# Kernel optimization log

Hardware: AMD Instinct MI355X
Metric: run time of the kernel (lower is better)

Reference implementation:

```python
import jax, jax.numpy as jnp
import numpy as np

NUM_JOINTS = 24
NUM_THETAS = NUM_JOINTS * 3  # 72
NUM_VERTS = 6890
NUM_BETAS = 10
BATCH = 512

SMPL_PARENTS = np.array([0, 0, 0, 0, 1, 2, 3, 4, 5, 6, 7, 8, 9, 9, 9,
                         12, 13, 14, 16, 17, 18, 19, 20, 21], dtype=np.int32)


def setup_inputs() -> dict:
    key = jax.random.key(0)
    ks = jax.random.split(key, 6)
    x = jax.random.normal(ks[0], (BATCH, NUM_THETAS + NUM_BETAS), dtype=jnp.float32) * 0.3
    v_template = jax.random.normal(ks[1], (NUM_VERTS, 3), dtype=jnp.float32) * 0.3
    shapedirs = jax.random.normal(ks[2], (NUM_BETAS, NUM_VERTS * 3), dtype=jnp.float32) * 0.01
    posedirs = jax.random.normal(ks[3], (207, NUM_VERTS * 3), dtype=jnp.float32) * 0.001
    Jr = jax.random.uniform(ks[4], (NUM_VERTS, NUM_JOINTS), dtype=jnp.float32)
    J_regressor = Jr / jnp.sum(Jr, axis=0, keepdims=True)
    W = jax.random.uniform(ks[5], (NUM_VERTS, NUM_JOINTS), dtype=jnp.float32)
    lbs_weights = W / jnp.sum(W, axis=1, keepdims=True)  # rows sum to 1 (skinning weights)
    parents = jnp.asarray(SMPL_PARENTS)
    return {"x": x, "v_template": v_template, "shapedirs": shapedirs,
            "J_regressor": J_regressor, "posedirs": posedirs,
            "lbs_weights": lbs_weights, "parents": parents}


def batch_rodrigues(theta):
    # theta: [N,3] axis-angle -> [N,3,3] rotation matrices
    angle = jnp.linalg.norm(theta + 1e-8, axis=1, keepdims=True)  # [N,1]
    r = theta / angle                                              # [N,3] unit axis
    cos = jnp.cos(angle)[..., None]                                # [N,1,1]
    sin = jnp.sin(angle)[..., None]
    outer = r[:, :, None] * r[:, None, :]                          # [N,3,3]
    rx, ry, rz = r[:, 0], r[:, 1], r[:, 2]
    zero = jnp.zeros_like(rx)
    K = jnp.stack([zero, -rz, ry,
                   rz, zero, -rx,
                   -ry, rx, zero], axis=1).reshape(-1, 3, 3)       # skew-symmetric
    eye = jnp.eye(3, dtype=theta.dtype)
    return cos * eye + (1.0 - cos) * outer + sin * K


def global_rigid_transformation(Rs, J, parents):
    # Rs: [B,24,3,3], J: [B,24,3] -> A: [B,24,4,4]
    B = Rs.shape[0]
    dtype = Rs.dtype
    bottom = jnp.broadcast_to(jnp.array([0, 0, 0, 1], dtype=dtype), (B, 1, 4))

    def make_A(R, t):  # R:[B,3,3], t:[B,3]
        Rt = jnp.concatenate([R, t[:, :, None]], axis=2)  # [B,3,4]
        return jnp.concatenate([Rt, bottom], axis=1)       # [B,4,4]

    parents = np.asarray(parents)
    results = [make_A(Rs[:, 0], J[:, 0])]
    for i in range(1, NUM_JOINTS):
        t_rel = J[:, i] - J[:, parents[i]]
        A_here = make_A(Rs[:, i], t_rel)
        results.append(jnp.matmul(results[parents[i]], A_here))
    results = jnp.stack(results, axis=1)  # [B,24,4,4]

    Js_w0 = jnp.concatenate([J, jnp.zeros((B, NUM_JOINTS, 1), dtype=dtype)], axis=2)  # [B,24,4]
    init_bone = jnp.einsum('bjpq,bjq->bjp', results, Js_w0)                           # [B,24,4]
    A = results - jnp.pad(init_bone[..., None], ((0, 0), (0, 0), (0, 0), (3, 0)))
    return A


def reference(x, v_template, shapedirs, J_regressor, posedirs, lbs_weights, parents):
    B = x.shape[0]
    thetas = x[:, :NUM_THETAS]
    betas = x[:, NUM_THETAS:]

    # shape blendshapes
    v_shaped = (betas @ shapedirs).reshape(B, NUM_VERTS, 3) + v_template  # [B,V,3]

    J = jnp.einsum('bvc,vj->bjc', v_shaped, J_regressor)  # [B,24,3]

    # pose rotations + pose blendshapes
    Rs = batch_rodrigues(thetas.reshape(-1, 3)).reshape(B, NUM_JOINTS, 3, 3)
    pose_feature = (Rs[:, 1:] - jnp.eye(3, dtype=x.dtype)).reshape(B, 207)
    v_posed = (pose_feature @ posedirs).reshape(B, NUM_VERTS, 3) + v_shaped

    # kinematic chain
    A = global_rigid_transformation(Rs, J, parents)  # [B,24,4,4]

    # linear blend skinning
    T = jnp.einsum('vj,bjpq->bvpq', lbs_weights, A)  # [B,V,4,4]
    v_posed_homo = jnp.concatenate(
        [v_posed, jnp.ones((B, NUM_VERTS, 1), dtype=x.dtype)], axis=2)  # [B,V,4]
    verts = jnp.einsum('bvpq,bvq->bvp', T, v_posed_homo)[:, :, :3]
    return verts
```

## Files before the change

kernel.cpp:

```cpp
#include <hip/hip_runtime.h>

#define NUM_JOINTS 24
#define NUM_VERTS  6890
#define NUM_COORDS (NUM_VERTS * 3)
#define NUM_BETAS  10
#define KTOT       217
#define KPAD       224
#define BATCH      512
#define NPAD       20672
#define DPAD       20736
#define VPAD       6912

#define WS_SJ   0
#define WS_JT   720
#define WS_XBF  800
#define WS_DBF  58144
#define WS_WHBF 2380576
#define WS_AH   2491168
#define WS_AL   2622240
#define WS_JRT  2753312

typedef __attribute__((ext_vector_type(8))) short short8;
typedef __attribute__((ext_vector_type(4))) float f32x4;

__device__ inline unsigned short f2bf(float f) {
    union { float f; unsigned u; } c; c.f = f;
    unsigned u = c.u;
    u += 0x7fffu + ((u >> 16) & 1u);
    return (unsigned short)(u >> 16);
}
__device__ inline float bf2f(unsigned short h) {
    union { unsigned u; float f; } c; c.u = ((unsigned)h) << 16;
    return c.f;
}

__global__ __launch_bounds__(256) void prep_vert(const float* __restrict__ Jr,
                                                 const float* __restrict__ w,
                                                 float* __restrict__ jrT,
                                                 unsigned short* __restrict__ whbf) {
    const int v = blockIdx.x * 256 + threadIdx.x;
    if (v >= VPAD) return;
    const bool ok = (v < NUM_VERTS);
    #pragma unroll
    for (int j = 0; j < 24; ++j)
        jrT[j * VPAD + v] = ok ? Jr[v * 24 + j] : 0.f;
    unsigned short row[32];
    #pragma unroll
    for (int j = 0; j < 32; ++j)
        row[j] = f2bf((ok && j < 24) ? w[v * 24 + j] : 0.f);
    #pragma unroll
    for (int i = 0; i < 4; ++i)
        *(float4*)(whbf + (size_t)v * 32 + i * 8) = *(const float4*)(&row[i * 8]);
}

__global__ __launch_bounds__(256) void reduce_sj(const float* __restrict__ jrT,
                                                 const float* __restrict__ sd,
                                                 const float* __restrict__ vt,
                                                 float* __restrict__ ws) {
    const int s = blockIdx.x;
    const int j = blockIdx.y;
    const int tid = threadIdx.x;
    const float* jr = jrT + j * VPAD;
    float sum = 0.f;
    if (s < 30) {
        const int k = s / 3, c = s % 3;
        const float* src = sd + (size_t)k * NUM_COORDS;
        for (int v = tid; v < NUM_VERTS; v += 256)
            sum += jr[v] * src[v * 3 + c];
    } else {
        const int c = s - 30;
        for (int v = tid; v < NUM_VERTS; v += 256)
            sum += jr[v] * vt[v * 3 + c];
    }
    __shared__ float red[256];
    red[tid] = sum;
    __syncthreads();
    for (int off = 128; off > 0; off >>= 1) {
        if (tid < off) red[tid] += red[tid + off];
        __syncthreads();
    }
    if (tid == 0) {
        if (s < 30) ws[WS_SJ + (s / 3) * 72 + j * 3 + (s % 3)] = red[0];
        else        ws[WS_JT + j * 3 + (s - 30)] = red[0];
    }
}

__global__ __launch_bounds__(256) void convert_dbf(const float* __restrict__ sd,
                                                   const float* __restrict__ pd,
                                                   unsigned short* __restrict__ dbf) {
    const int c = blockIdx.x * 256 + threadIdx.x;
    const bool valid = (c < NUM_COORDS);
    unsigned short* drow = dbf + (size_t)c * KPAD;
    for (int g = 0; g < 4; ++g) {
        unsigned buf[28];
        #pragma unroll
        for (int h = 0; h < 28; ++h) {
            const int k0 = g * 56 + 2 * h;
            const int k1 = k0 + 1;
            float v0 = 0.f, v1 = 0.f;
            if (valid) {
                v0 = (k0 < 10) ? sd[(size_t)k0 * NUM_COORDS + c]
                   : (k0 < KTOT) ? pd[(size_t)(k0 - 10) * NUM_COORDS + c] : 0.f;
                v1 = (k1 < 10) ? sd[(size_t)k1 * NUM_COORDS + c]
                   : (k1 < KTOT) ? pd[(size_t)(k1 - 10) * NUM_COORDS + c] : 0.f;
            }
            buf[h] = (unsigned)f2bf(v0) | ((unsigned)f2bf(v1) << 16);
        }
        #pragma unroll
        for (int h = 0; h < 7; ++h)
            *(float4*)(drow + g * 56 + h * 8) = *(const float4*)(&buf[h * 4]);
    }
}

__global__ __launch_bounds__(64) void per_batch(const float* __restrict__ x,
                                                const int* __restrict__ parents,
                                                const float* __restrict__ ws_sj,
                                                unsigned short* __restrict__ ahi,
                                                unsigned short* __restrict__ alo,
                                                unsigned short* __restrict__ xbf) {
    const int b = blockIdx.x;
    const int tid = threadIdx.x;
    __shared__ float Rs[24][9], Jl[24][3], Rg[24][9], tg[24][3], As[24][12];
    const float* row = x + b * (NUM_BETAS + 72);

    if (tid < 24) {
        const int j = tid;
        const float t0 = row[3 * j + 0], t1 = row[3 * j + 1], t2 = row[3 * j + 2];
        const float a0 = t0 + 1e-8f, a1 = t1 + 1e-8f, a2 = t2 + 1e-8f;
        const float angle = sqrtf(a0 * a0 + a1 * a1 + a2 * a2);
        const float inv = 1.0f / angle;
        const float rx = t0 * inv, ry = t1 * inv, rz = t2 * inv;
        const float c = cosf(angle), sn = sinf(angle), o = 1.f - c;
        float R[9];
        R[0] = c + o * rx * rx;       R[1] = o * rx * ry - sn * rz; R[2] = o * rx * rz + sn * ry;
        R[3] = o * rx * ry + sn * rz; R[4] = c + o * ry * ry;       R[5] = o * ry * rz - sn * rx;
        R[6] = o * rx * rz - sn * ry; R[7] = o * ry * rz + sn * rx; R[8] = c + o * rz * rz;
        #pragma unroll
        for (int i = 0; i < 9; ++i) Rs[j][i] = R[i];
        #pragma unroll
        for (int c3 = 0; c3 < 3; ++c3) {
            float s = ws_sj[WS_JT + j * 3 + c3];
            #pragma unroll
            for (int k = 0; k < NUM_BETAS; ++k)
                s += row[72 + k] * ws_sj[WS_SJ + k * 72 + j * 3 + c3];
            Jl[j][c3] = s;
        }
        if (j >= 1) {
            #pragma unroll
            for (int i = 0; i < 9; ++i) {
                const float pf = R[i] - ((i == 0 || i == 4 || i == 8) ? 1.f : 0.f);
                xbf[(size_t)b * KPAD + 10 + (j - 1) * 9 + i] = f2bf(pf);
            }
        }
    }
    if (tid < NUM_BETAS) xbf[(size_t)b * KPAD + tid] = f2bf(row[72 + tid]);
    if (tid == 63) {
        #pragma unroll
        for (int k = KTOT; k < KPAD; ++k) xbf[(size_t)b * KPAD + k] = 0;
    }
    __syncthreads();

    if (tid == 0) {
        #pragma unroll
        for (int i = 0; i < 9; ++i) Rg[0][i] = Rs[0][i];
        #pragma unroll
        for (int c3 = 0; c3 < 3; ++c3) tg[0][c3] = Jl[0][c3];
        for (int i = 1; i < 24; ++i) {
            const int p = parents[i];
            float tmp[9];
            #pragma unroll
            for (int r = 0; r < 3; ++r)
                #pragma unroll
                for (int cc = 0; cc < 3; ++cc)
                    tmp[r * 3 + cc] = Rg[p][r * 3 + 0] * Rs[i][0 + cc] +
                                      Rg[p][r * 3 + 1] * Rs[i][3 + cc] +
                                      Rg[p][r * 3 + 2] * Rs[i][6 + cc];
            #pragma unroll
            for (int q = 0; q < 9; ++q) Rg[i][q] = tmp[q];
            const float tr0 = Jl[i][0] - Jl[p][0];
            const float tr1 = Jl[i][1] - Jl[p][1];
            const float tr2 = Jl[i][2] - Jl[p][2];
            #pragma unroll
            for (int r = 0; r < 3; ++r)
                tg[i][r] = Rg[p][r * 3 + 0] * tr0 + Rg[p][r * 3 + 1] * tr1 +
                           Rg[p][r * 3 + 2] * tr2 + tg[p][r];
        }
    }
    __syncthreads();

    if (tid < 24) {
        const int j = tid;
        #pragma unroll
        for (int r = 0; r < 3; ++r) {
            const float t = tg[j][r] - (Rg[j][r * 3 + 0] * Jl[j][0] +
                                        Rg[j][r * 3 + 1] * Jl[j][1] +
                                        Rg[j][r * 3 + 2] * Jl[j][2]);
            As[j][r * 4 + 0] = Rg[j][r * 3 + 0];
            As[j][r * 4 + 1] = Rg[j][r * 3 + 1];
            As[j][r * 4 + 2] = Rg[j][r * 3 + 2];
            As[j][r * 4 + 3] = t;
        }
    }
    __syncthreads();

    if (tid < 32) {
        const int r = tid >> 1;
        const int half = tid & 1;
        unsigned short hi[16], lo[16];
        #pragma unroll
        for (int i = 0; i < 16; ++i) {
            const int j = half * 16 + i;
            float v = 0.f;
            if (r < 12 && j < 24) v = As[j][r];
            const unsigned short h = f2bf(v);
            hi[i] = h;
            lo[i] = f2bf(v - bf2f(h));
        }
        unsigned short* dh = ahi + ((size_t)b * 16 + r) * 32 + half * 16;
        unsigned short* dl = alo + ((size_t)b * 16 + r) * 32 + half * 16;
        #pragma unroll
        for (int i = 0; i < 2; ++i) {
            *(float4*)(dh + i * 8) = *(const float4*)(&hi[i * 8]);
            *(float4*)(dl + i * 8) = *(const float4*)(&lo[i * 8]);
        }
    }
}

__global__ __launch_bounds__(256) void gemm_mfma(const unsigned short* __restrict__ dbf,
                                                 const unsigned short* __restrict__ xbf,
                                                 const float* __restrict__ vt,
                                                 float* __restrict__ out) {
    __shared__ __align__(16) unsigned short Xs[64 * 232];
    const int tid  = threadIdx.x;
    const int wave = tid >> 6;
    const int lane = tid & 63;
    const int col  = lane & 15;
    const int quad = lane >> 4;
    const int n0   = blockIdx.x * 64;
    const int nc   = n0 + wave * 16 + col;

    short8 bfrag[7];
    {
        const unsigned short* brow = dbf + (size_t)nc * KPAD + quad * 8;
        #pragma unroll
        for (int kb = 0; kb < 7; ++kb)
            bfrag[kb] = *(const short8*)(brow + kb * 32);
    }
    const float vtl = (nc < NUM_COORDS) ? vt[nc] : 0.f;
    const bool nok = (nc < NUM_COORDS);

    for (int chunk = 0; chunk < 2; ++chunk) {
        const int m0 = blockIdx.y * 128 + chunk * 64;
        __syncthreads();
        #pragma unroll
        for (int i = 0; i < 7; ++i) {
            const int c = tid + i * 256;
            const int r = c / 28;
            const int off = c % 28;
            const float4 v = *(const float4*)(xbf + (size_t)(m0 + r) * KPAD + off * 8);
            *(float4*)(&Xs[r * 232 + off * 8]) = v;
        }
        __syncthreads();

        #pragma unroll
        for (int mt = 0; mt < 4; ++mt) {
            const unsigned short* arow = &Xs[(mt * 16 + col) * 232 + quad * 8];
            f32x4 acc = {0.f, 0.f, 0.f, 0.f};
            #pragma unroll
            for (int kb = 0; kb < 7; ++kb) {
                const short8 afrag = *(const short8*)(arow + kb * 32);
                acc = __builtin_amdgcn_mfma_f32_16x16x32_bf16(afrag, bfrag[kb], acc, 0, 0, 0);
            }
            if (nok) {
                float* base = out + (size_t)(m0 + mt * 16 + quad * 4) * NUM_COORDS + nc;
                base[0]                       = acc[0] + vtl;
                base[(size_t)NUM_COORDS]      = acc[1] + vtl;
                base[(size_t)2 * NUM_COORDS]  = acc[2] + vtl;
                base[(size_t)3 * NUM_COORDS]  = acc[3] + vtl;
            }
        }
    }
}

__global__ __launch_bounds__(256) void skin_mfma(const unsigned short* __restrict__ whbf,
                                                 const unsigned short* __restrict__ ahi,
                                                 const unsigned short* __restrict__ alo,
                                                 float* __restrict__ out) {
    __shared__ float Ts[4][64 * 17];
    const int tid  = threadIdx.x;
    const int wave = tid >> 6;
    const int lane = tid & 63;
    const int col  = lane & 15;
    const int quad = lane >> 4;
    const int v0   = blockIdx.x * 64;
    const int b0   = blockIdx.y * 32;

    short8 wfrag[4];
    #pragma unroll
    for (int mt = 0; mt < 4; ++mt)
        wfrag[mt] = *(const short8*)(whbf + (size_t)(v0 + mt * 16 + col) * 32 + quad * 8);

    float* ts = &Ts[wave][0];
    const int vv = v0 + lane;
    const bool vok = (vv < NUM_VERTS);

    for (int nt = wave; nt < 32; nt += 4) {
        const int b = b0 + nt;
        float* orow = out + (size_t)b * NUM_COORDS + (size_t)vv * 3;
        float h0 = 0.f, h1 = 0.f, h2 = 0.f;
        if (vok) { h0 = orow[0]; h1 = orow[1]; h2 = orow[2]; }

        const short8 bh = *(const short8*)(ahi + ((size_t)b * 16 + col) * 32 + quad * 8);
        const short8 bl = *(const short8*)(alo + ((size_t)b * 16 + col) * 32 + quad * 8);

        f32x4 acc[4];
        #pragma unroll
        for (int mt = 0; mt < 4; ++mt) {
            f32x4 z = {0.f, 0.f, 0.f, 0.f};
            z = __builtin_amdgcn_mfma_f32_16x16x32_bf16(wfrag[mt], bh, z, 0, 0, 0);
            z = __builtin_amdgcn_mfma_f32_16x16x32_bf16(wfrag[mt], bl, z, 0, 0, 0);
            acc[mt] = z;
        }
        #pragma unroll
        for (int mt = 0; mt < 4; ++mt)
            #pragma unroll
            for (int r = 0; r < 4; ++r)
                ts[(mt * 16 + quad * 4 + r) * 17 + col] = acc[mt][r];

        float Tp[12];
        #pragma unroll
        for (int i = 0; i < 12; ++i) Tp[i] = ts[lane * 17 + i];

        if (vok) {
            const float o0 = Tp[0] * h0 + Tp[1] * h1 + Tp[2]  * h2 + Tp[3];
            const float o1 = Tp[4] * h0 + Tp[5] * h1 + Tp[6]  * h2 + Tp[7];
            const float o2 = Tp[8] * h0 + Tp[9] * h1 + Tp[10] * h2 + Tp[11];
            orow[0] = o0; orow[1] = o1; orow[2] = o2;
        }
    }
}

extern "C" void kernel_launch(void* const* d_in, const int* in_sizes, int n_in,
                              void* d_out, int out_size, void* d_ws, size_t ws_size,
                              hipStream_t stream) {
    const float* x  = (const float*)d_in[0];
    const float* vt = (const float*)d_in[1];
    const float* sd = (const float*)d_in[2];
    const float* Jr = (const float*)d_in[3];
    const float* pd = (const float*)d_in[4];
    const float* w  = (const float*)d_in[5];
    const int* parents = (const int*)d_in[6];
    float* out = (float*)d_out;
    float* ws  = (float*)d_ws;
    unsigned short* xbf  = (unsigned short*)(ws + WS_XBF);
    unsigned short* dbf  = (unsigned short*)(ws + WS_DBF);
    unsigned short* whbf = (unsigned short*)(ws + WS_WHBF);
    unsigned short* ahi  = (unsigned short*)(ws + WS_AH);
    unsigned short* alo  = (unsigned short*)(ws + WS_AL);
    float* jrT = ws + WS_JRT;

    prep_vert  <<<27, 256, 0, stream>>>(Jr, w, jrT, whbf);
    convert_dbf<<<81, 256, 0, stream>>>(sd, pd, dbf);
    reduce_sj  <<<dim3(33, 24), 256, 0, stream>>>(jrT, sd, vt, ws);
    per_batch  <<<BATCH, 64, 0, stream>>>(x, parents, ws, ahi, alo, xbf);
    gemm_mfma  <<<dim3(323, 4), 256, 0, stream>>>(dbf, xbf, vt, out);
    skin_mfma  <<<dim3(108, 16), 256, 0, stream>>>(whbf, ahi, alo, out);
}
```

Measured before the change: 165.6 us.

## Fuse all stages into one cooperative persistent kernel with grid syncs

Replaces the six separate launches with a single cooperative kernel that runs the prep, per-batch, GEMM and skinning stages as tile loops separated by grid-wide syncs. Four non-cooperative kernels remain as a fallback. The joint-regressor transpose buffer is dropped, so the reduction now reads Jr directly with a strided access. The per-batch stage packs four batches into each 256-thread block. The aim is to remove launch gaps between stages, at the cost of grid.sync overhead, a grid size capped at 1024 blocks, and host-side occupancy and attribute queries on every call.

```diff
diff --git a/kernel.cpp b/kernel.cpp
--- a/kernel.cpp
+++ b/kernel.cpp
@@ -1,4 +1,7 @@
 #include <hip/hip_runtime.h>
+#include <hip/hip_cooperative_groups.h>
+
+namespace cg = cooperative_groups;
 
 #define NUM_JOINTS 24
 #define NUM_VERTS  6890
@@ -7,8 +10,6 @@
 #define KTOT       217
 #define KPAD       224
 #define BATCH      512
-#define NPAD       20672
-#define DPAD       20736
 #define VPAD       6912
 
 #define WS_SJ   0
@@ -18,7 +19,6 @@
 #define WS_WHBF 2380576
 #define WS_AH   2491168
 #define WS_AL   2622240
-#define WS_JRT  2753312
 
 typedef __attribute__((ext_vector_type(8))) short short8;
 typedef __attribute__((ext_vector_type(4))) float f32x4;
@@ -34,97 +34,103 @@
     return c.f;
 }
 
-__global__ __launch_bounds__(256) void prep_vert(const float* __restrict__ Jr,
-                                                 const float* __restrict__ w,
-                                                 float* __restrict__ jrT,
-                                                 unsigned short* __restrict__ whbf) {
-    const int v = blockIdx.x * 256 + threadIdx.x;
-    if (v >= VPAD) return;
-    const bool ok = (v < NUM_VERTS);
-    #pragma unroll
-    for (int j = 0; j < 24; ++j)
-        jrT[j * VPAD + v] = ok ? Jr[v * 24 + j] : 0.f;
-    unsigned short row[32];
-    #pragma unroll
-    for (int j = 0; j < 32; ++j)
-        row[j] = f2bf((ok && j < 24) ? w[v * 24 + j] : 0.f);
-    #pragma unroll
-    for (int i = 0; i < 4; ++i)
-        *(float4*)(whbf + (size_t)v * 32 + i * 8) = *(const float4*)(&row[i * 8]);
-}
-
-__global__ __launch_bounds__(256) void reduce_sj(const float* __restrict__ jrT,
-                                                 const float* __restrict__ sd,
-                                                 const float* __restrict__ vt,
-                                                 float* __restrict__ ws) {
-    const int s = blockIdx.x;
-    const int j = blockIdx.y;
-    const int tid = threadIdx.x;
-    const float* jr = jrT + j * VPAD;
-    float sum = 0.f;
-    if (s < 30) {
-        const int k = s / 3, c = s % 3;
-        const float* src = sd + (size_t)k * NUM_COORDS;
-        for (int v = tid; v < NUM_VERTS; v += 256)
-            sum += jr[v] * src[v * 3 + c];
+struct PBShm {
+    float Rs[4][24][9];
+    float Jl[4][24][3];
+    float Rg[4][24][9];
+    float tg[4][24][3];
+    float As[4][24][12];
+};
+
+
+__device__ __forceinline__ void tile_prep(int t, int tid,
+                                          const float* __restrict__ Jr,
+                                          const float* __restrict__ sd,
+                                          const float* __restrict__ pd,
+                                          const float* __restrict__ vt,
+                                          const float* __restrict__ w,
+                                          unsigned short* __restrict__ whbf,
+                                          unsigned short* __restrict__ dbf,
+                                          float* __restrict__ ws,
+                                          float* red) {
+    if (t < 27) {
+        const int v = t * 256 + tid;
+        const bool ok = (v < NUM_VERTS);
+        unsigned short row[32];
+        #pragma unroll
+        for (int j = 0; j < 32; ++j)
+            row[j] = f2bf((ok && j < 24) ? w[v * 24 + j] : 0.f);
+        #pragma unroll
+        for (int i = 0; i < 4; ++i)
+            *(float4*)(whbf + (size_t)v * 32 + i * 8) = *(const float4*)(&row[i * 8]);
+    } else if (t < 108) {
+        const int c = (t - 27) * 256 + tid;
+        const bool valid = (c < NUM_COORDS);
+        unsigned short* drow = dbf + (size_t)c * KPAD;
+        for (int g = 0; g < 4; ++g) {
+            unsigned buf[28];
+            #pragma unroll
+            for (int h = 0; h < 28; ++h) {
+                const int k0 = g * 56 + 2 * h;
+                const int k1 = k0 + 1;
+                float v0 = 0.f, v1 = 0.f;
+                if (valid) {
+                    v0 = (k0 < 10) ? sd[(size_t)k0 * NUM_COORDS + c]
+                       : (k0 < KTOT) ? pd[(size_t)(k0 - 10) * NUM_COORDS + c] : 0.f;
+                    v1 = (k1 < 10) ? sd[(size_t)k1 * NUM_COORDS + c]
+                       : (k1 < KTOT) ? pd[(size_t)(k1 - 10) * NUM_COORDS + c] : 0.f;
+                }
+                buf[h] = (unsigned)f2bf(v0) | ((unsigned)f2bf(v1) << 16);
+            }
+            #pragma unroll
+            for (int h = 0; h < 7; ++h)
+                *(float4*)(drow + g * 56 + h * 8) = *(const float4*)(&buf[h * 4]);
+        }
     } else {
-        const int c = s - 30;
-        for (int v = tid; v < NUM_VERTS; v += 256)
-            sum += jr[v] * vt[v * 3 + c];
-    }
-    __shared__ float red[256];
-    red[tid] = sum;
-    __syncthreads();
-    for (int off = 128; off > 0; off >>= 1) {
-        if (tid < off) red[tid] += red[tid + off];
+        const int u = t - 108;
+        const int s = u % 33;
+        const int j = u / 33;
+        float sum = 0.f;
+        if (s < 30) {
+            const int k = s / 3, c = s % 3;
+            const float* src = sd + (size_t)k * NUM_COORDS;
+            for (int v = tid; v < NUM_VERTS; v += 256)
+                sum += Jr[v * 24 + j] * src[v * 3 + c];
+        } else {
+            const int c = s - 30;
+            for (int v = tid; v < NUM_VERTS; v += 256)
+                sum += Jr[v * 24 + j] * vt[v * 3 + c];
+        }
+        red[tid] = sum;
         __syncthreads();
-    }
-    if (tid == 0) {
-        if (s < 30) ws[WS_SJ + (s / 3) * 72 + j * 3 + (s % 3)] = red[0];
-        else        ws[WS_JT + j * 3 + (s - 30)] = red[0];
-    }
-}
-
-__global__ __launch_bounds__(256) void convert_dbf(const float* __restrict__ sd,
-                                                   const float* __restrict__ pd,
-                                                   unsigned short* __restrict__ dbf) {
-    const int c = blockIdx.x * 256 + threadIdx.x;
-    const bool valid = (c < NUM_COORDS);
-    unsigned short* drow = dbf + (size_t)c * KPAD;
-    for (int g = 0; g < 4; ++g) {
-        unsigned buf[28];
-        #pragma unroll
-        for (int h = 0; h < 28; ++h) {
-            const int k0 = g * 56 + 2 * h;
-            const int k1 = k0 + 1;
-            float v0 = 0.f, v1 = 0.f;
-            if (valid) {
-                v0 = (k0 < 10) ? sd[(size_t)k0 * NUM_COORDS + c]
-                   : (k0 < KTOT) ? pd[(size_t)(k0 - 10) * NUM_COORDS + c] : 0.f;
-                v1 = (k1 < 10) ? sd[(size_t)k1 * NUM_COORDS + c]
-                   : (k1 < KTOT) ? pd[(size_t)(k1 - 10) * NUM_COORDS + c] : 0.f;
-            }
-            buf[h] = (unsigned)f2bf(v0) | ((unsigned)f2bf(v1) << 16);
-        }
-        #pragma unroll
-        for (int h = 0; h < 7; ++h)
-            *(float4*)(drow + g * 56 + h * 8) = *(const float4*)(&buf[h * 4]);
-    }
-}
-
-__global__ __launch_bounds__(64) void per_batch(const float* __restrict__ x,
-                                                const int* __restrict__ parents,
-                                                const float* __restrict__ ws_sj,
-                                                unsigned short* __restrict__ ahi,
-                                                unsigned short* __restrict__ alo,
-                                                unsigned short* __restrict__ xbf) {
-    const int b = blockIdx.x;
-    const int tid = threadIdx.x;
-    __shared__ float Rs[24][9], Jl[24][3], Rg[24][9], tg[24][3], As[24][12];
+        for (int off = 128; off > 0; off >>= 1) {
+            if (tid < off) red[tid] += red[tid + off];
+            __syncthreads();
+        }
+        if (tid == 0) {
+            if (s < 30) ws[WS_SJ + (s / 3) * 72 + j * 3 + (s % 3)] = red[0];
+            else        ws[WS_JT + j * 3 + (s - 30)] = red[0];
+        }
+        __syncthreads();
+    }
+}
+
+__device__ __forceinline__ void tile_pb(int t, int tid,
+                                        const float* __restrict__ x,
+                                        const int* __restrict__ parents,
+                                        float* __restrict__ ws,
+                                        unsigned short* __restrict__ ahi,
+                                        unsigned short* __restrict__ alo,
+                                        unsigned short* __restrict__ xbf,
+                                        PBShm* Pp) {
+    PBShm& P = *Pp;
+    const int sub  = tid >> 6;
+    const int lane = tid & 63;
+    const int b = t * 4 + sub;
     const float* row = x + b * (NUM_BETAS + 72);
 
-    if (tid < 24) {
-        const int j = tid;
+    if (lane < 24) {
+        const int j = lane;
         const float t0 = row[3 * j + 0], t1 = row[3 * j + 1], t2 = row[3 * j + 2];
         const float a0 = t0 + 1e-8f, a1 = t1 + 1e-8f, a2 = t2 + 1e-8f;
         const float angle = sqrtf(a0 * a0 + a1 * a1 + a2 * a2);
@@ -136,14 +142,14 @@
         R[3] = o * rx * ry + sn * rz; R[4] = c + o * ry * ry;       R[5] = o * ry * rz - sn * rx;
         R[6] = o * rx * rz - sn * ry; R[7] = o * ry * rz + sn * rx; R[8] = c + o * rz * rz;
         #pragma unroll
-        for (int i = 0; i < 9; ++i) Rs[j][i] = R[i];
+        for (int i = 0; i < 9; ++i) P.Rs[sub][j][i] = R[i];
         #pragma unroll
         for (int c3 = 0; c3 < 3; ++c3) {
-            float s = ws_sj[WS_JT + j * 3 + c3];
+            float s = ws[WS_JT + j * 3 + c3];
             #pragma unroll
             for (int k = 0; k < NUM_BETAS; ++k)
-                s += row[72 + k] * ws_sj[WS_SJ + k * 72 + j * 3 + c3];
-            Jl[j][c3] = s;
+                s += row[72 + k] * ws[WS_SJ + k * 72 + j * 3 + c3];
+            P.Jl[sub][j][c3] = s;
         }
         if (j >= 1) {
             #pragma unroll
@@ -153,18 +159,18 @@
             }
         }
     }
-    if (tid < NUM_BETAS) xbf[(size_t)b * KPAD + tid] = f2bf(row[72 + tid]);
-    if (tid == 63) {
+    if (lane < NUM_BETAS) xbf[(size_t)b * KPAD + lane] = f2bf(row[72 + lane]);
+    if (lane == 63) {
         #pragma unroll
         for (int k = KTOT; k < KPAD; ++k) xbf[(size_t)b * KPAD + k] = 0;
     }
     __syncthreads();
 
-    if (tid == 0) {
-        #pragma unroll
-        for (int i = 0; i < 9; ++i) Rg[0][i] = Rs[0][i];
-        #pragma unroll
-        for (int c3 = 0; c3 < 3; ++c3) tg[0][c3] = Jl[0][c3];
+    if (lane == 0) {
+        #pragma unroll
+        for (int i = 0; i < 9; ++i) P.Rg[sub][0][i] = P.Rs[sub][0][i];
+        #pragma unroll
+        for (int c3 = 0; c3 < 3; ++c3) P.tg[sub][0][c3] = P.Jl[sub][0][c3];
         for (int i = 1; i < 24; ++i) {
             const int p = parents[i];
             float tmp[9];
@@ -172,46 +178,46 @@
             for (int r = 0; r < 3; ++r)
                 #pragma unroll
                 for (int cc = 0; cc < 3; ++cc)
-                    tmp[r * 3 + cc] = Rg[p][r * 3 + 0] * Rs[i][0 + cc] +
-                                      Rg[p][r * 3 + 1] * Rs[i][3 + cc] +
-                                      Rg[p][r * 3 + 2] * Rs[i][6 + cc];
-            #pragma unroll
-            for (int q = 0; q < 9; ++q) Rg[i][q] = tmp[q];
-            const float tr0 = Jl[i][0] - Jl[p][0];
-            const float tr1 = Jl[i][1] - Jl[p][1];
-            const float tr2 = Jl[i][2] - Jl[p][2];
+                    tmp[r * 3 + cc] = P.Rg[sub][p][r * 3 + 0] * P.Rs[sub][i][0 + cc] +
+                                      P.Rg[sub][p][r * 3 + 1] * P.Rs[sub][i][3 + cc] +
+                                      P.Rg[sub][p][r * 3 + 2] * P.Rs[sub][i][6 + cc];
+            #pragma unroll
+            for (int q = 0; q < 9; ++q) P.Rg[sub][i][q] = tmp[q];
+            const float tr0 = P.Jl[sub][i][0] - P.Jl[sub][p][0];
+            const float tr1 = P.Jl[sub][i][1] - P.Jl[sub][p][1];
+            const float tr2 = P.Jl[sub][i][2] - P.Jl[sub][p][2];
             #pragma unroll
             for (int r = 0; r < 3; ++r)
-                tg[i][r] = Rg[p][r * 3 + 0] * tr0 + Rg[p][r * 3 + 1] * tr1 +
-                           Rg[p][r * 3 + 2] * tr2 + tg[p][r];
+                P.tg[sub][i][r] = P.Rg[sub][p][r * 3 + 0] * tr0 + P.Rg[sub][p][r * 3 + 1] * tr1 +
+                                  P.Rg[sub][p][r * 3 + 2] * tr2 + P.tg[sub][p][r];
         }
     }
     __syncthreads();
 
-    if (tid < 24) {
-        const int j = tid;
+    if (lane < 24) {
+        const int j = lane;
         #pragma unroll
         for (int r = 0; r < 3; ++r) {
-            const float t = tg[j][r] - (Rg[j][r * 3 + 0] * Jl[j][0] +
-                                        Rg[j][r * 3 + 1] * Jl[j][1] +
-                                        Rg[j][r * 3 + 2] * Jl[j][2]);
-            As[j][r * 4 + 0] = Rg[j][r * 3 + 0];
-            As[j][r * 4 + 1] = Rg[j][r * 3 + 1];
-            As[j][r * 4 + 2] = Rg[j][r * 3 + 2];
-            As[j][r * 4 + 3] = t;
+            const float tt = P.tg[sub][j][r] - (P.Rg[sub][j][r * 3 + 0] * P.Jl[sub][j][0] +
+                                                P.Rg[sub][j][r * 3 + 1] * P.Jl[sub][j][1] +
+                                                P.Rg[sub][j][r * 3 + 2] * P.Jl[sub][j][2]);
+            P.As[sub][j][r * 4 + 0] = P.Rg[sub][j][r * 3 + 0];
+            P.As[sub][j][r * 4 + 1] = P.Rg[sub][j][r * 3 + 1];
+            P.As[sub][j][r * 4 + 2] = P.Rg[sub][j][r * 3 + 2];
+            P.As[sub][j][r * 4 + 3] = tt;
         }
     }
     __syncthreads();
 
-    if (tid < 32) {
-        const int r = tid >> 1;
-        const int half = tid & 1;
+    if (lane < 32) {
+        const int r = lane >> 1;
+        const int half = lane & 1;
         unsigned short hi[16], lo[16];
         #pragma unroll
         for (int i = 0; i < 16; ++i) {
             const int j = half * 16 + i;
             float v = 0.f;
-            if (r < 12 && j < 24) v = As[j][r];
+            if (r < 12 && j < 24) v = P.As[sub][j][r];
             const unsigned short h = f2bf(v);
             hi[i] = h;
             lo[i] = f2bf(v - bf2f(h));
@@ -224,19 +230,20 @@
             *(float4*)(dl + i * 8) = *(const float4*)(&lo[i * 8]);
         }
     }
-}
-
-__global__ __launch_bounds__(256) void gemm_mfma(const unsigned short* __restrict__ dbf,
-                                                 const unsigned short* __restrict__ xbf,
-                                                 const float* __restrict__ vt,
-                                                 float* __restrict__ out) {
-    __shared__ __align__(16) unsigned short Xs[64 * 232];
-    const int tid  = threadIdx.x;
+    __syncthreads();
+}
+
+__device__ __forceinline__ void tile_gemm(int txx, int tyy, int tid,
+                                          const unsigned short* __restrict__ dbf,
+                                          const unsigned short* __restrict__ xbf,
+                                          const float* __restrict__ vt,
+                                          float* __restrict__ out,
+                                          unsigned short* Xs) {
     const int wave = tid >> 6;
     const int lane = tid & 63;
     const int col  = lane & 15;
     const int quad = lane >> 4;
-    const int n0   = blockIdx.x * 64;
+    const int n0   = txx * 64;
     const int nc   = n0 + wave * 16 + col;
 
     short8 bfrag[7];
@@ -250,7 +257,7 @@
     const bool nok = (nc < NUM_COORDS);
 
     for (int chunk = 0; chunk < 2; ++chunk) {
-        const int m0 = blockIdx.y * 128 + chunk * 64;
+        const int m0 = tyy * 128 + chunk * 64;
         __syncthreads();
         #pragma unroll
         for (int i = 0; i < 7; ++i) {
@@ -280,27 +287,28 @@
             }
         }
     }
-}
-
-__global__ __launch_bounds__(256) void skin_mfma(const unsigned short* __restrict__ whbf,
-                                                 const unsigned short* __restrict__ ahi,
-                                                 const unsigned short* __restrict__ alo,
-                                                 float* __restrict__ out) {
-    __shared__ float Ts[4][64 * 17];
-    const int tid  = threadIdx.x;
+    __syncthreads();
+}
+
+__device__ __forceinline__ void tile_skin(int txx, int tyy, int tid,
+                                          const unsigned short* __restrict__ whbf,
+                                          const unsigned short* __restrict__ ahi,
+                                          const unsigned short* __restrict__ alo,
+                                          float* __restrict__ out,
+                                          float* Tsf) {
     const int wave = tid >> 6;
     const int lane = tid & 63;
     const int col  = lane & 15;
     const int quad = lane >> 4;
-    const int v0   = blockIdx.x * 64;
-    const int b0   = blockIdx.y * 32;
+    const int v0   = txx * 64;
+    const int b0   = tyy * 32;
+    float* ts = Tsf + wave * (64 * 17);
 
     short8 wfrag[4];
     #pragma unroll
     for (int mt = 0; mt < 4; ++mt)
         wfrag[mt] = *(const short8*)(whbf + (size_t)(v0 + mt * 16 + col) * 32 + quad * 8);
 
-    float* ts = &Ts[wave][0];
     const int vv = v0 + lane;
     const bool vok = (vv < NUM_VERTS);
 
@@ -338,6 +346,76 @@
             orow[0] = o0; orow[1] = o1; orow[2] = o2;
         }
     }
+}
+
+__global__ __launch_bounds__(256) void mega(const float* __restrict__ x,
+                                            const float* __restrict__ vt,
+                                            const float* __restrict__ sd,
+                                            const float* __restrict__ Jr,
+                                            const float* __restrict__ pd,
+                                            const float* __restrict__ w,
+                                            const int* __restrict__ parents,
+                                            float* __restrict__ out,
+                                            float* __restrict__ ws) {
+    __shared__ __align__(16) unsigned char smem[29696];
+    unsigned short* xbf  = (unsigned short*)(ws + WS_XBF);
+    unsigned short* dbf  = (unsigned short*)(ws + WS_DBF);
+    unsigned short* whbf = (unsigned short*)(ws + WS_WHBF);
+    unsigned short* ahi  = (unsigned short*)(ws + WS_AH);
+    unsigned short* alo  = (unsigned short*)(ws + WS_AL);
+
+    cg::grid_group grid = cg::this_grid();
+    const int tid = threadIdx.x;
+    const int bx  = blockIdx.x;
+    const int GS  = gridDim.x;
+
+    for (int t = bx; t < 900; t += GS)
+        tile_prep(t, tid, Jr, sd, pd, vt, w, whbf, dbf, ws, (float*)smem);
+    grid.sync();
+    for (int t = bx; t < 128; t += GS)
+        tile_pb(t, tid, x, parents, ws, ahi, alo, xbf, (PBShm*)smem);
+    grid.sync();
+    for (int t = bx; t < 1292; t += GS)
+        tile_gemm(t % 323, t / 323, tid, dbf, xbf, vt, out, (unsigned short*)smem);
+    grid.sync();
+    for (int t = bx; t < 1728; t += GS)
+        tile_skin(t % 108, t / 108, tid, whbf, ahi, alo, out, (float*)smem);
+}
+
+__global__ __launch_bounds__(256) void k_prep(const float* __restrict__ Jr,
+                                              const float* __restrict__ sd,
+                                              const float* __restrict__ pd,
+                                              const float* __restrict__ vt,
+                                              const float* __restrict__ w,
+                                              float* __restrict__ ws) {
+    __shared__ float red[256];
+    tile_prep(blockIdx.x, threadIdx.x, Jr, sd, pd, vt, w,
+              (unsigned short*)(ws + WS_WHBF), (unsigned short*)(ws + WS_DBF), ws, red);
+}
+
+__global__ __launch_bounds__(256) void k_pb(const float* __restrict__ x,
+                                            const int* __restrict__ parents,
+                                            float* __restrict__ ws) {
+    __shared__ PBShm P;
+    tile_pb(blockIdx.x, threadIdx.x, x, parents, ws,
+            (unsigned short*)(ws + WS_AH), (unsigned short*)(ws + WS_AL),
+            (unsigned short*)(ws + WS_XBF), &P);
+}
+
+__global__ __launch_bounds__(256) void k_gemm(const float* __restrict__ vt,
+                                              float* __restrict__ out,
+                                              float* __restrict__ ws) {
+    __shared__ __align__(16) unsigned short Xs[64 * 232];
+    tile_gemm(blockIdx.x, blockIdx.y, threadIdx.x,
+              (unsigned short*)(ws + WS_DBF), (unsigned short*)(ws + WS_XBF), vt, out, Xs);
+}
+
+__global__ __launch_bounds__(256) void k_skin(float* __restrict__ out,
+                                              float* __restrict__ ws) {
+    __shared__ float Ts[4 * 64 * 17];
+    tile_skin(blockIdx.x, blockIdx.y, threadIdx.x,
+              (unsigned short*)(ws + WS_WHBF), (unsigned short*)(ws + WS_AH),
+              (unsigned short*)(ws + WS_AL), out, Ts);
 }
 
 extern "C" void kernel_launch(void* const* d_in, const int* in_sizes, int n_in,
@@ -352,17 +430,28 @@
     const int* parents = (const int*)d_in[6];
     float* out = (float*)d_out;
     float* ws  = (float*)d_ws;
-    unsigned short* xbf  = (unsigned short*)(ws + WS_XBF);
-    unsigned short* dbf  = (unsigned short*)(ws + WS_DBF);
-    unsigned short* whbf = (unsigned short*)(ws + WS_WHBF);
-    unsigned short* ahi  = (unsigned short*)(ws + WS_AH);
-    unsigned short* alo  = (unsigned short*)(ws + WS_AL);
-    float* jrT = ws + WS_JRT;
-
-    prep_vert  <<<27, 256, 0, stream>>>(Jr, w, jrT, whbf);
-    convert_dbf<<<81, 256, 0, stream>>>(sd, pd, dbf);
-    reduce_sj  <<<dim3(33, 24), 256, 0, stream>>>(jrT, sd, vt, ws);
-    per_batch  <<<BATCH, 64, 0, stream>>>(x, parents, ws, ahi, alo, xbf);
-    gemm_mfma  <<<dim3(323, 4), 256, 0, stream>>>(dbf, xbf, vt, out);
-    skin_mfma  <<<dim3(108, 16), 256, 0, stream>>>(whbf, ahi, alo, out);
-}
+
+    int dev = 0;
+    hipGetDevice(&dev);
+    int coop = 0;
+    hipDeviceGetAttribute(&coop, hipDeviceAttributeCooperativeLaunch, dev);
+    int nb = 0;
+    hipOccupancyMaxActiveBlocksPerMultiprocessor(&nb, reinterpret_cast<const void*>(mega), 256, 0);
+
+    bool launched = false;
+    if (coop && nb > 0) {
+        int gridsz = nb * 256;
+        if (gridsz > 1024) gridsz = 1024;
+        void* kargs[] = {(void*)&x, (void*)&vt, (void*)&sd, (void*)&Jr, (void*)&pd,
+                         (void*)&w, (void*)&parents, (void*)&out, (void*)&ws};
+        hipError_t e = hipLaunchCooperativeKernel(reinterpret_cast<void*>(mega),
+                                                  dim3(gridsz), dim3(256), kargs, 0, stream);
+        launched = (e == hipSuccess);
+    }
+    if (!launched) {
+        k_prep<<<900, 256, 0, stream>>>(Jr, sd, pd, vt, w, ws);
+        k_pb  <<<128, 256, 0, stream>>>(x, parents, ws);
+        k_gemm<<<dim3(323, 4), 256, 0, stream>>>(vt, out, ws);
+        k_skin<<<dim3(108, 16), 256, 0, stream>>>(out, ws);
+    }
+}
```

Result: slower. 290.2 us (+75.2%).
